# Kernel optimization log

Measured on AMD Instinct MI355X. Metric: run time of the kernel, lower is better.

The kernel has to match this reference:

```python
import jax, jax.numpy as jnp
import numpy as np

B, S, D, Q, N, H = 2, 2048, 4096, 32, 8, 128
ROPE_THETA = 10000.0


def apply_rope(x, positions, head_dim, theta):
    # x: [B, S, heads, H], positions: [B, S] int
    half = head_dim // 2
    inv_freq = 1.0 / (theta ** (jnp.arange(half, dtype=jnp.float32) * 2.0 / head_dim))
    angles = positions.astype(jnp.float32)[..., None] * inv_freq  # [B, S, half]
    cos = jnp.cos(angles)[:, :, None, :]  # [B, S, 1, half]
    sin = jnp.sin(angles)[:, :, None, :]
    x1, x2 = x[..., :half], x[..., half:]
    return jnp.concatenate([x1 * cos - x2 * sin, x2 * cos + x1 * sin], axis=-1).astype(x.dtype)


def setup_inputs() -> dict:
    key = jax.random.key(0)
    ks = jax.random.split(key, 5)
    x = jax.random.normal(ks[0], (B, S, D), dtype=jnp.float32)
    positions = jnp.broadcast_to(jnp.arange(S, dtype=jnp.int32)[None, :], (B, S))
    scale = 0.02
    Wq = jax.random.normal(ks[1], (Q, D, H), dtype=jnp.float32) * scale
    Wk = jax.random.normal(ks[2], (N, D, H), dtype=jnp.float32) * scale
    Wv = jax.random.normal(ks[3], (N, D, H), dtype=jnp.float32) * scale
    Wo = jax.random.normal(ks[4], (Q, H, D), dtype=jnp.float32) * scale
    return {"x": x, "positions": positions, "Wq": Wq, "Wk": Wk, "Wv": Wv, "Wo": Wo}


def reference(x, positions, Wq, Wk, Wv, Wo):
    # Prefill path: QKV proj + RoPE + GQA causal attention + O proj.
    head_repeats = Q // N
    q_BSQH = jnp.einsum('BSD,QDH->BSQH', x, Wq)
    q_BSQH = apply_rope(q_BSQH, positions, H, ROPE_THETA)
    k_BSNH = jnp.einsum('BSD,NDH->BSNH', x, Wk)
    k_BSNH = apply_rope(k_BSNH, positions, H, ROPE_THETA)
    v_BSNH = jnp.einsum('BSD,NDH->BSNH', x, Wv)
    # GQA head repeat
    k_BTQH = jnp.repeat(k_BSNH, head_repeats, axis=2) if head_repeats > 1 else k_BSNH
    v_BTQH = jnp.repeat(v_BSNH, head_repeats, axis=2) if head_repeats > 1 else v_BSNH
    scores_BQST = jnp.einsum('BSQH,BTQH->BQST', q_BSQH, k_BTQH) / jnp.sqrt(jnp.float32(H))
    causal = jnp.tril(jnp.ones((1, 1, S, S), dtype=jnp.bool_))
    scores_BQST = jnp.where(causal, scores_BQST, -jnp.inf)
    weights_BQST = jax.nn.softmax(scores_BQST, axis=-1)
    out_BSQH = jnp.einsum('BQST,BTQH->BSQH', weights_BQST, v_BTQH)
    o_BSD = jnp.einsum('BSQH,QHD->BSD', out_BSQH, Wo)
    return o_BSD
```

## Files before the change

### kernel.cpp

```cpp
#include <hip/hip_runtime.h>
#include <cstdint>
#include <cstddef>

#define B_  2
#define S_  2048
#define D_  4096
#define QH_ 32
#define NH_ 8
#define HD_ 128
#define MROWS (B_ * S_)
#define NQKV  (QH_ * HD_ + 2 * NH_ * HD_)
#define KOFF  (QH_ * HD_)
#define VOFF  (QH_ * HD_ + NH_ * HD_)

typedef __attribute__((ext_vector_type(8))) short bf16x8;
typedef __attribute__((ext_vector_type(4))) float f32x4;

__device__ __forceinline__ unsigned short f2bf(float f) {
    unsigned int u = __float_as_uint(f);
    return (unsigned short)((u + 0x7FFFu + ((u >> 16) & 1u)) >> 16);
}
__device__ __forceinline__ float bf2f(unsigned short h) { return __uint_as_float(((unsigned int)h) << 16); }

__device__ __forceinline__ void gl2lds16(const void* g, void* l) {
    __builtin_amdgcn_global_load_lds(
        (const __attribute__((address_space(1))) void*)g,
        (__attribute__((address_space(3))) void*)l, 16, 0, 0);
}

__global__ __launch_bounds__(256)
void convert_bf16_kernel(const float* __restrict__ in, unsigned short* __restrict__ out)
{
    const size_t i = ((size_t)blockIdx.x * 256 + threadIdx.x) * 8;
    float4 a = *(const float4*)(in + i);
    float4 b = *(const float4*)(in + i + 4);
    uint4 o;
    o.x = (unsigned int)f2bf(a.x) | ((unsigned int)f2bf(a.y) << 16);
    o.y = (unsigned int)f2bf(a.z) | ((unsigned int)f2bf(a.w) << 16);
    o.z = (unsigned int)f2bf(b.x) | ((unsigned int)f2bf(b.y) << 16);
    o.w = (unsigned int)f2bf(b.z) | ((unsigned int)f2bf(b.w) << 16);
    *(uint4*)(out + i) = o;
}

__global__ __launch_bounds__(256)
void transpose_conv_kernel(const float* __restrict__ in, unsigned short* __restrict__ out,
                           int R, int C)
{
    __shared__ unsigned short tile[64][72];
    const int t  = threadIdx.x;
    const int c0 = blockIdx.x * 64;
    const int r0 = blockIdx.y * 64;
    in  += (size_t)blockIdx.z * R * C;
    out += (size_t)blockIdx.z * R * C;
    {
        const int rr = t >> 4;
        const int cc = (t & 15) * 4;
        #pragma unroll
        for (int p = 0; p < 4; ++p) {
            float4 v = *(const float4*)(in + (size_t)(r0 + p * 16 + rr) * C + c0 + cc);
            unsigned int lo = (unsigned int)f2bf(v.x) | ((unsigned int)f2bf(v.y) << 16);
            unsigned int hi = (unsigned int)f2bf(v.z) | ((unsigned int)f2bf(v.w) << 16);
            *(uint2*)&tile[p * 16 + rr][cc] = make_uint2(lo, hi);
        }
    }
    __syncthreads();
    {
        const int j  = t >> 3;
        const int i8 = (t & 7) * 8;
        #pragma unroll
        for (int p = 0; p < 2; ++p) {
            unsigned short tmp[8];
            #pragma unroll
            for (int e = 0; e < 8; ++e) tmp[e] = tile[i8 + e][p * 32 + j];
            *(uint4*)(out + (size_t)(c0 + p * 32 + j) * R + r0 + i8) = *(uint4*)tmp;
        }
    }
}

__global__ __launch_bounds__(256)
void transpose_v_kernel(const unsigned short* __restrict__ qkv, unsigned short* __restrict__ vt)
{
    __shared__ unsigned short tile[64][76];
    const int t  = threadIdx.x;
    const int z  = blockIdx.z;
    const int b  = z >> 3, kh = z & 7;
    const int h0 = blockIdx.x * 64;
    const int s0 = blockIdx.y * 64;
    const unsigned short* in = qkv + (size_t)(b * S_) * NQKV + VOFF + kh * HD_;
    unsigned short* outb = vt + (size_t)z * HD_ * S_;
    {
        const int rr = t >> 4;
        const int cc = (t & 15) * 4;
        #pragma unroll
        for (int p = 0; p < 4; ++p) {
            uint2 v = *(const uint2*)(in + (size_t)(s0 + p * 16 + rr) * NQKV + h0 + cc);
            *(uint2*)&tile[p * 16 + rr][cc] = v;
        }
    }
    __syncthreads();
    {
        const int j  = t >> 3;
        const int i8 = (t & 7) * 8;
        #pragma unroll
        for (int p = 0; p < 2; ++p) {
            unsigned short tmp[8];
            #pragma unroll
            for (int e = 0; e < 8; ++e) tmp[e] = tile[i8 + e][p * 32 + j];
            *(uint4*)(outb + (size_t)(h0 + p * 32 + j) * S_ + s0 + i8) = *(uint4*)tmp;
        }
    }
}

template<int CF32>
__global__ __launch_bounds__(512, 2)
void gemm256_kernel(const unsigned short* __restrict__ A,
                    const unsigned short* __restrict__ Bt,
                    void* __restrict__ Cp, int Nst, int K)
{
    __shared__ alignas(16) unsigned short lds[3][2][256][32];

    const int t = threadIdx.x, l = t & 63, w = t >> 6;
    const int gx  = gridDim.x;
    const int nwg = gx * gridDim.y;
    int lin = blockIdx.y * gx + blockIdx.x;
    lin = (lin & 7) * (nwg >> 3) + (lin >> 3);
    const int bn = (lin % gx) * 256, bm = (lin / gx) * 256;
    const int wr = w >> 2, wc = w & 3;
    const int lm = l & 15, lg = l >> 4;

    f32x4 acc[8][4];
    #pragma unroll
    for (int i = 0; i < 8; ++i)
        #pragma unroll
        for (int j = 0; j < 4; ++j) acc[i][j] = (f32x4){0.f, 0.f, 0.f, 0.f};

    const int srow = w * 16 + (l >> 2);
    const int scol = (l & 3) * 8;
    const unsigned short* Asrc = A  + (size_t)(bm + srow) * K + scol;
    const unsigned short* Bsrc = Bt + (size_t)(bn + srow) * K + scol;

    #define STAGE_A(tt, bb) do {                                                  \
        gl2lds16(Asrc + (size_t)(tt) * 32,                  &lds[bb][0][w*16][0]); \
        gl2lds16(Asrc + (size_t)128*K + (size_t)(tt) * 32,  &lds[bb][0][128 + w*16][0]); } while (0)
    #define STAGE_B(tt, bb) do {                                                  \
        gl2lds16(Bsrc + (size_t)(tt) * 32,                  &lds[bb][1][w*16][0]); \
        gl2lds16(Bsrc + (size_t)128*K + (size_t)(tt) * 32,  &lds[bb][1][128 + w*16][0]); } while (0)

    const int nkt = K >> 5;
    STAGE_A(0, 0); STAGE_B(0, 0);
    STAGE_A(1, 1); STAGE_B(1, 1);

    for (int kt = 0; kt < nkt; ++kt) {
        if (kt + 1 < nkt) asm volatile("s_waitcnt vmcnt(4)" ::: "memory");
        else              asm volatile("s_waitcnt vmcnt(0)" ::: "memory");
        asm volatile("s_barrier" ::: "memory");

        const unsigned short (*bufA)[32] = lds[kt % 3][0];
        const unsigned short (*bufB)[32] = lds[kt % 3][1];
        const int nb = (kt + 2) % 3;

        bf16x8 bfr[4], afr[4];
        #pragma unroll
        for (int j = 0; j < 4; ++j) bfr[j] = *(const bf16x8*)&bufB[wc * 64 + j * 16 + lm][lg * 8];
        #pragma unroll
        for (int i = 0; i < 4; ++i) afr[i] = *(const bf16x8*)&bufA[wr * 128 + i * 16 + lm][lg * 8];
        if (kt + 2 < nkt) STAGE_A(kt + 2, nb);
        __builtin_amdgcn_s_setprio(1);
        #pragma unroll
        for (int i = 0; i < 4; ++i)
            #pragma unroll
            for (int j = 0; j < 4; ++j)
                acc[i][j] = __builtin_amdgcn_mfma_f32_16x16x32_bf16(afr[i], bfr[j], acc[i][j], 0, 0, 0);
        __builtin_amdgcn_s_setprio(0);
        asm volatile("s_barrier" ::: "memory");

        #pragma unroll
        for (int i = 0; i < 4; ++i) afr[i] = *(const bf16x8*)&bufA[wr * 128 + (i + 4) * 16 + lm][lg * 8];
        if (kt + 2 < nkt) STAGE_B(kt + 2, nb);
        __builtin_amdgcn_s_setprio(1);
        #pragma unroll
        for (int i = 0; i < 4; ++i)
            #pragma unroll
            for (int j = 0; j < 4; ++j)
                acc[i + 4][j] = __builtin_amdgcn_mfma_f32_16x16x32_bf16(afr[i], bfr[j], acc[i + 4][j], 0, 0, 0);
        __builtin_amdgcn_s_setprio(0);
    }
    #undef STAGE_A
    #undef STAGE_B

    const int lr4 = lg * 4;
    #pragma unroll
    for (int i = 0; i < 8; ++i) {
        #pragma unroll
        for (int j = 0; j < 4; ++j) {
            int row = bm + wr * 128 + i * 16 + lr4;
            int col = bn + wc * 64 + j * 16 + lm;
            #pragma unroll
            for (int jj = 0; jj < 4; ++jj) {
                if constexpr (CF32)
                    ((float*)Cp)[(size_t)(row + jj) * Nst + col] = acc[i][j][jj];
                else
                    ((unsigned short*)Cp)[(size_t)(row + jj) * Nst + col] = f2bf(acc[i][j][jj]);
            }
        }
    }
}

template<int LOG2H>
__global__ __launch_bounds__(256)
void rope_kernel(unsigned short* __restrict__ data, const int* __restrict__ positions)
{
    const int gid  = blockIdx.x * 256 + threadIdx.x;
    const int j    = gid & 63;
    const int hr   = gid >> 6;
    const int head = hr & ((1 << LOG2H) - 1);
    const int bs   = hr >> LOG2H;
    const float pos = (float)positions[bs];
    const float inv = expf(-0.14391156831f * (float)j);
    float s, c;
    sincosf(pos * inv, &s, &c);
    const size_t base = (size_t)bs * NQKV + head * HD_;
    const float x1 = bf2f(data[base + j]);
    const float x2 = bf2f(data[base + 64 + j]);
    data[base + j]      = f2bf(x1 * c - x2 * s);
    data[base + 64 + j] = f2bf(x2 * c + x1 * s);
}

__global__ __launch_bounds__(256)
void attn_kernel(const unsigned short* __restrict__ qkv,
                 const unsigned short* __restrict__ vt,
                 unsigned short* __restrict__ ao)
{
    constexpr int LDK = 136;
    constexpr int LDV = 72;
    __shared__ alignas(16) unsigned short k_s[64][LDK];
    __shared__ alignas(16) unsigned short v_t[128][LDV];
    __shared__ alignas(16) unsigned short p_s[4][16][LDV];

    const int t   = threadIdx.x;
    const int blk = blockIdx.x;
    const int sb  = 31 - (blk >> 6);
    const int pr  = blk & 63;
    const int qh  = pr >> 1;
    const int b   = pr & 1;
    const int kh  = qh >> 2;
    const int l   = t & 63, w = t >> 6;
    const int lm  = l & 15;
    const int lg  = l >> 4;
    const int lg4 = lg * 4;
    const int lko = lg * 8;
    const int wrow = w * 16 + lm;

    const unsigned short* vtb = vt + (size_t)(b * NH_ + kh) * HD_ * S_;

    bf16x8 qf[4];
    {
        const size_t qrow = (size_t)(b * S_ + sb * 64 + wrow) * NQKV + qh * HD_;
        #pragma unroll
        for (int kk = 0; kk < 4; ++kk)
            qf[kk] = *(const bf16x8*)(qkv + qrow + kk * 32 + lko);
    }

    f32x4 acc_o[8];
    #pragma unroll
    for (int i = 0; i < 8; ++i) acc_o[i] = (f32x4){0.f, 0.f, 0.f, 0.f};
    float mreg = -1e30f, lreg = 0.f;

    const float sm_scale = 0.08838834764831845f;

    for (int c = 0; c <= sb; ++c) {
        __syncthreads();
        {
            const int key = t >> 2, seg = t & 3;
            const size_t g = (size_t)(b * S_ + c * 64 + key) * NQKV + KOFF + kh * HD_ + seg * 32;
            const uint4* ksrc = (const uint4*)(qkv + g);
            #pragma unroll
            for (int i = 0; i < 4; ++i)
                *(uint4*)&k_s[key][seg * 32 + i * 8] = ksrc[i];
        }
        {
            const int h  = t >> 1;
            const int ko = (t & 1) * 32;
            const unsigned short* src = vtb + (size_t)h * S_ + c * 64 + ko;
            #pragma unroll
            for (int i = 0; i < 4; ++i)
                *(uint4*)&v_t[h][ko + i * 8] = *(const uint4*)(src + i * 8);
        }
        __syncthreads();

        f32x4 acc_s[4];
        #pragma unroll
        for (int t4 = 0; t4 < 4; ++t4) acc_s[t4] = (f32x4){0.f, 0.f, 0.f, 0.f};
        #pragma unroll
        for (int kk = 0; kk < 4; ++kk) {
            const bf16x8 qv = qf[kk];
            bf16x8 kf0 = *(const bf16x8*)&k_s[0 * 16 + lm][kk * 32 + lko];
            bf16x8 kf1 = *(const bf16x8*)&k_s[1 * 16 + lm][kk * 32 + lko];
            bf16x8 kf2 = *(const bf16x8*)&k_s[2 * 16 + lm][kk * 32 + lko];
            bf16x8 kf3 = *(const bf16x8*)&k_s[3 * 16 + lm][kk * 32 + lko];
            __builtin_amdgcn_s_setprio(1);
            acc_s[0] = __builtin_amdgcn_mfma_f32_16x16x32_bf16(kf0, qv, acc_s[0], 0, 0, 0);
            acc_s[1] = __builtin_amdgcn_mfma_f32_16x16x32_bf16(kf1, qv, acc_s[1], 0, 0, 0);
            acc_s[2] = __builtin_amdgcn_mfma_f32_16x16x32_bf16(kf2, qv, acc_s[2], 0, 0, 0);
            acc_s[3] = __builtin_amdgcn_mfma_f32_16x16x32_bf16(kf3, qv, acc_s[3], 0, 0, 0);
            __builtin_amdgcn_s_setprio(0);
        }

        const bool diag = (c == sb);
        float p[4][4];
        #pragma unroll
        for (int t4 = 0; t4 < 4; ++t4)
            #pragma unroll
            for (int r = 0; r < 4; ++r) {
                float s = acc_s[t4][r] * sm_scale;
                if (diag && (t4 * 16 + lg4 + r > wrow)) s = -1e30f;
                p[t4][r] = s;
            }
        float mc = p[0][0];
        #pragma unroll
        for (int t4 = 0; t4 < 4; ++t4)
            #pragma unroll
            for (int r = 0; r < 4; ++r) mc = fmaxf(mc, p[t4][r]);
        mc = fmaxf(mc, __shfl_xor(mc, 16, 64));
        mc = fmaxf(mc, __shfl_xor(mc, 32, 64));
        float sf = 1.0f;
        if (mc > mreg + 8.0f) {
            sf = __expf(mreg - mc);
            mreg = mc;
            lreg *= sf;
        }
        if (__any(sf != 1.0f)) {
            #pragma unroll
            for (int r = 0; r < 4; ++r) {
                const float s_r = __shfl(sf, (l & 48) | (lg4 + r), 64);
                #pragma unroll
                for (int ht = 0; ht < 8; ++ht) acc_o[ht][r] *= s_r;
            }
        }
        float ps = 0.f;
        #pragma unroll
        for (int t4 = 0; t4 < 4; ++t4)
            #pragma unroll
            for (int r = 0; r < 4; ++r) {
                p[t4][r] = __expf(p[t4][r] - mreg);
                ps += p[t4][r];
            }
        ps += __shfl_xor(ps, 16, 64);
        ps += __shfl_xor(ps, 32, 64);
        lreg += ps;
        #pragma unroll
        for (int t4 = 0; t4 < 4; ++t4) {
            unsigned int d0 = (unsigned int)f2bf(p[t4][0]) | ((unsigned int)f2bf(p[t4][1]) << 16);
            unsigned int d1 = (unsigned int)f2bf(p[t4][2]) | ((unsigned int)f2bf(p[t4][3]) << 16);
            *(unsigned int*)&p_s[w][lm][t4 * 16 + lg4]     = d0;
            *(unsigned int*)&p_s[w][lm][t4 * 16 + lg4 + 2] = d1;
        }

        #pragma unroll
        for (int kk = 0; kk < 2; ++kk) {
            const bf16x8 pa = *(const bf16x8*)&p_s[w][lm][kk * 32 + lko];
            #pragma unroll
            for (int ht = 0; ht < 8; ht += 4) {
                bf16x8 bv0 = *(const bf16x8*)&v_t[(ht + 0) * 16 + lm][kk * 32 + lko];
                bf16x8 bv1 = *(const bf16x8*)&v_t[(ht + 1) * 16 + lm][kk * 32 + lko];
                bf16x8 bv2 = *(const bf16x8*)&v_t[(ht + 2) * 16 + lm][kk * 32 + lko];
                bf16x8 bv3 = *(const bf16x8*)&v_t[(ht + 3) * 16 + lm][kk * 32 + lko];
                __builtin_amdgcn_s_setprio(1);
                acc_o[ht + 0] = __builtin_amdgcn_mfma_f32_16x16x32_bf16(pa, bv0, acc_o[ht + 0], 0, 0, 0);
                acc_o[ht + 1] = __builtin_amdgcn_mfma_f32_16x16x32_bf16(pa, bv1, acc_o[ht + 1], 0, 0, 0);
                acc_o[ht + 2] = __builtin_amdgcn_mfma_f32_16x16x32_bf16(pa, bv2, acc_o[ht + 2], 0, 0, 0);
                acc_o[ht + 3] = __builtin_amdgcn_mfma_f32_16x16x32_bf16(pa, bv3, acc_o[ht + 3], 0, 0, 0);
                __builtin_amdgcn_s_setprio(0);
            }
        }
    }

    #pragma unroll
    for (int r = 0; r < 4; ++r) {
        const float lr = __shfl(lreg, (l & 48) | (lg4 + r), 64);
        const float invl = 1.f / lr;
        const size_t row = (size_t)(b * S_ + sb * 64 + w * 16 + lg4 + r);
        #pragma unroll
        for (int ht = 0; ht < 8; ++ht)
            ao[(row * QH_ + qh) * HD_ + ht * 16 + lm] = f2bf(acc_o[ht][r] * invl);
    }
}

extern "C" void kernel_launch(void* const* d_in, const int* in_sizes, int n_in,
                              void* d_out, int out_size, void* d_ws, size_t ws_size,
                              hipStream_t stream)
{
    const float* x  = (const float*)d_in[0];
    const int*  pos = (const int*)d_in[1];
    const float* Wq = (const float*)d_in[2];
    const float* Wk = (const float*)d_in[3];
    const float* Wv = (const float*)d_in[4];
    const float* Wo = (const float*)d_in[5];
    float* out = (float*)d_out;

    char* wsb = (char*)d_ws;
    unsigned short* qkv = (unsigned short*)(wsb);
    unsigned short* wt  = (unsigned short*)(wsb + 50331648);
    unsigned short* vt  = (unsigned short*)(wsb + 83886080);
    unsigned short* r0  = (unsigned short*)(wsb + 100663296);

    const dim3 blk(256);
    const dim3 blk512(512);
    convert_bf16_kernel<<<8192, blk, 0, stream>>>(x, r0);
    transpose_conv_kernel<<<dim3(2, 64, 32), blk, 0, stream>>>(Wq, wt, D_, HD_);
    transpose_conv_kernel<<<dim3(2, 64, 8),  blk, 0, stream>>>(Wk, wt + (size_t)KOFF * D_, D_, HD_);
    transpose_conv_kernel<<<dim3(2, 64, 8),  blk, 0, stream>>>(Wv, wt + (size_t)VOFF * D_, D_, HD_);
    gemm256_kernel<0><<<dim3(NQKV / 256, MROWS / 256), blk512, 0, stream>>>(r0, wt, qkv, NQKV, D_);
    transpose_conv_kernel<<<dim3(64, 64, 1), blk, 0, stream>>>(Wo, wt, D_, D_);
    transpose_v_kernel<<<dim3(2, 32, 16), blk, 0, stream>>>(qkv, vt);
    rope_kernel<5><<<(MROWS * QH_ * 64) / 256, blk, 0, stream>>>(qkv, pos);
    rope_kernel<3><<<(MROWS * NH_ * 64) / 256, blk, 0, stream>>>(qkv + KOFF, pos);
    attn_kernel<<<B_ * QH_ * (S_ / 64), blk, 0, stream>>>(qkv, vt, r0);
    gemm256_kernel<1><<<dim3(D_ / 256, MROWS / 256), blk512, 0, stream>>>(r0, wt, out, D_, QH_ * HD_);
}
```

Before: 607.2 us.

## Rewrite GEMM as 8-phase ping-pong pipeline with 64-wide K tiles and swizzled LDS

```diff
diff --git a/kernel.cpp b/kernel.cpp
--- a/kernel.cpp
+++ b/kernel.cpp
@@ -113,11 +113,12 @@
 
 template<int CF32>
 __global__ __launch_bounds__(512, 2)
-void gemm256_kernel(const unsigned short* __restrict__ A,
-                    const unsigned short* __restrict__ Bt,
-                    void* __restrict__ Cp, int Nst, int K)
-{
-    __shared__ alignas(16) unsigned short lds[3][2][256][32];
+void gemm8p_kernel(const unsigned short* __restrict__ A,
+                   const unsigned short* __restrict__ Bt,
+                   void* __restrict__ Cp, int Nst, int K)
+{
+    __shared__ alignas(16) unsigned short Al[2][2][128][64];
+    __shared__ alignas(16) unsigned short Bl[2][2][128][64];
 
     const int t = threadIdx.x, l = t & 63, w = t >> 6;
     const int gx  = gridDim.x;
@@ -128,73 +129,134 @@
     const int wr = w >> 2, wc = w & 3;
     const int lm = l & 15, lg = l >> 4;
 
+    const int sk  = ((lm >> 2) & 1) << 5;
+    const int kc0 = sk + lg * 8;
+    const int kc1 = (sk ^ 32) + lg * 8;
+
     f32x4 acc[8][4];
     #pragma unroll
     for (int i = 0; i < 8; ++i)
         #pragma unroll
         for (int j = 0; j < 4; ++j) acc[i][j] = (f32x4){0.f, 0.f, 0.f, 0.f};
 
-    const int srow = w * 16 + (l >> 2);
-    const int scol = (l & 3) * 8;
-    const unsigned short* Asrc = A  + (size_t)(bm + srow) * K + scol;
-    const unsigned short* Bsrc = Bt + (size_t)(bn + srow) * K + scol;
-
-    #define STAGE_A(tt, bb) do {                                                  \
-        gl2lds16(Asrc + (size_t)(tt) * 32,                  &lds[bb][0][w*16][0]); \
-        gl2lds16(Asrc + (size_t)128*K + (size_t)(tt) * 32,  &lds[bb][0][128 + w*16][0]); } while (0)
-    #define STAGE_B(tt, bb) do {                                                  \
-        gl2lds16(Bsrc + (size_t)(tt) * 32,                  &lds[bb][1][w*16][0]); \
-        gl2lds16(Bsrc + (size_t)128*K + (size_t)(tt) * 32,  &lds[bb][1][128 + w*16][0]); } while (0)
-
-    const int nkt = K >> 5;
-    STAGE_A(0, 0); STAGE_B(0, 0);
-    STAGE_A(1, 1); STAGE_B(1, 1);
+    const int srow = w * 8 + (l >> 3);
+    const int scol = (((l & 7) ^ (((l >> 5) & 1) << 2))) * 8;
+    const unsigned short* Ag = A  + (size_t)(bm + srow) * K + scol;
+    const unsigned short* Bg = Bt + (size_t)(bn + srow) * K + scol;
+
+    #define STG_A(bb, hh, ko) do { \
+        gl2lds16(Ag + (size_t)((hh) * 128) * K + (ko),      &Al[bb][hh][w * 8][0]);      \
+        gl2lds16(Ag + (size_t)((hh) * 128 + 64) * K + (ko), &Al[bb][hh][64 + w * 8][0]); } while (0)
+    #define STG_B(bb, hh, ko) do { \
+        gl2lds16(Bg + (size_t)((hh) * 128) * K + (ko),      &Bl[bb][hh][w * 8][0]);      \
+        gl2lds16(Bg + (size_t)((hh) * 128 + 64) * K + (ko), &Bl[bb][hh][64 + w * 8][0]); } while (0)
+
+    const int nkt = K >> 6;
+    STG_A(0, 0, 0); STG_B(0, 0, 0); STG_B(0, 1, 0); STG_A(0, 1, 0);
+    asm volatile("s_waitcnt vmcnt(4)" ::: "memory");
+    asm volatile("s_barrier" ::: "memory");
+
+    bf16x8 af[4][2], bfp[2][2];
 
     for (int kt = 0; kt < nkt; ++kt) {
-        if (kt + 1 < nkt) asm volatile("s_waitcnt vmcnt(4)" ::: "memory");
-        else              asm volatile("s_waitcnt vmcnt(0)" ::: "memory");
-        asm volatile("s_barrier" ::: "memory");
-
-        const unsigned short (*bufA)[32] = lds[kt % 3][0];
-        const unsigned short (*bufB)[32] = lds[kt % 3][1];
-        const int nb = (kt + 2) % 3;
-
-        bf16x8 bfr[4], afr[4];
-        #pragma unroll
-        for (int j = 0; j < 4; ++j) bfr[j] = *(const bf16x8*)&bufB[wc * 64 + j * 16 + lm][lg * 8];
-        #pragma unroll
-        for (int i = 0; i < 4; ++i) afr[i] = *(const bf16x8*)&bufA[wr * 128 + i * 16 + lm][lg * 8];
-        if (kt + 2 < nkt) STAGE_A(kt + 2, nb);
+        const int cur = kt & 1, nxt = cur ^ 1;
+        const bool pf = (kt + 1 < nkt);
+        const size_t ko = (size_t)(kt + 1) * 64;
+        const unsigned short (*Ac0)[64] = Al[cur][0];
+        const unsigned short (*Ac1)[64] = Al[cur][1];
+        const unsigned short (*Bc0)[64] = Bl[cur][0];
+        const unsigned short (*Bc1)[64] = Bl[cur][1];
+
+        #pragma unroll
+        for (int i = 0; i < 4; ++i) {
+            af[i][0] = *(const bf16x8*)&Ac0[wr * 16 + i * 32 + lm][kc0];
+            af[i][1] = *(const bf16x8*)&Ac0[wr * 16 + i * 32 + lm][kc1];
+        }
+        #pragma unroll
+        for (int j = 0; j < 2; ++j) {
+            bfp[j][0] = *(const bf16x8*)&Bc0[j * 64 + wc * 16 + lm][kc0];
+            bfp[j][1] = *(const bf16x8*)&Bc0[j * 64 + wc * 16 + lm][kc1];
+        }
+        if (pf) STG_A(nxt, 0, ko);
+        asm volatile("s_barrier" ::: "memory");
         __builtin_amdgcn_s_setprio(1);
         #pragma unroll
         for (int i = 0; i < 4; ++i)
             #pragma unroll
-            for (int j = 0; j < 4; ++j)
-                acc[i][j] = __builtin_amdgcn_mfma_f32_16x16x32_bf16(afr[i], bfr[j], acc[i][j], 0, 0, 0);
+            for (int j = 0; j < 2; ++j) {
+                acc[i][j] = __builtin_amdgcn_mfma_f32_16x16x32_bf16(af[i][0], bfp[j][0], acc[i][j], 0, 0, 0);
+                acc[i][j] = __builtin_amdgcn_mfma_f32_16x16x32_bf16(af[i][1], bfp[j][1], acc[i][j], 0, 0, 0);
+            }
         __builtin_amdgcn_s_setprio(0);
-        asm volatile("s_barrier" ::: "memory");
-
-        #pragma unroll
-        for (int i = 0; i < 4; ++i) afr[i] = *(const bf16x8*)&bufA[wr * 128 + (i + 4) * 16 + lm][lg * 8];
-        if (kt + 2 < nkt) STAGE_B(kt + 2, nb);
+        asm volatile("s_waitcnt vmcnt(4)" ::: "memory");
+        asm volatile("s_barrier" ::: "memory");
+
+        #pragma unroll
+        for (int j = 0; j < 2; ++j) {
+            bfp[j][0] = *(const bf16x8*)&Bc1[j * 64 + wc * 16 + lm][kc0];
+            bfp[j][1] = *(const bf16x8*)&Bc1[j * 64 + wc * 16 + lm][kc1];
+        }
+        if (pf) STG_B(nxt, 0, ko);
+        asm volatile("s_barrier" ::: "memory");
         __builtin_amdgcn_s_setprio(1);
         #pragma unroll
         for (int i = 0; i < 4; ++i)
             #pragma unroll
-            for (int j = 0; j < 4; ++j)
-                acc[i + 4][j] = __builtin_amdgcn_mfma_f32_16x16x32_bf16(afr[i], bfr[j], acc[i + 4][j], 0, 0, 0);
+            for (int j = 0; j < 2; ++j) {
+                acc[i][j + 2] = __builtin_amdgcn_mfma_f32_16x16x32_bf16(af[i][0], bfp[j][0], acc[i][j + 2], 0, 0, 0);
+                acc[i][j + 2] = __builtin_amdgcn_mfma_f32_16x16x32_bf16(af[i][1], bfp[j][1], acc[i][j + 2], 0, 0, 0);
+            }
         __builtin_amdgcn_s_setprio(0);
-    }
-    #undef STAGE_A
-    #undef STAGE_B
+        asm volatile("s_waitcnt vmcnt(4)" ::: "memory");
+        asm volatile("s_barrier" ::: "memory");
+
+        #pragma unroll
+        for (int i = 0; i < 4; ++i) {
+            af[i][0] = *(const bf16x8*)&Ac1[wr * 16 + i * 32 + lm][kc0];
+            af[i][1] = *(const bf16x8*)&Ac1[wr * 16 + i * 32 + lm][kc1];
+        }
+        if (pf) STG_B(nxt, 1, ko);
+        asm volatile("s_barrier" ::: "memory");
+        __builtin_amdgcn_s_setprio(1);
+        #pragma unroll
+        for (int i = 0; i < 4; ++i)
+            #pragma unroll
+            for (int j = 0; j < 2; ++j) {
+                acc[i + 4][j + 2] = __builtin_amdgcn_mfma_f32_16x16x32_bf16(af[i][0], bfp[j][0], acc[i + 4][j + 2], 0, 0, 0);
+                acc[i + 4][j + 2] = __builtin_amdgcn_mfma_f32_16x16x32_bf16(af[i][1], bfp[j][1], acc[i + 4][j + 2], 0, 0, 0);
+            }
+        __builtin_amdgcn_s_setprio(0);
+        asm volatile("s_barrier" ::: "memory");
+
+        #pragma unroll
+        for (int j = 0; j < 2; ++j) {
+            bfp[j][0] = *(const bf16x8*)&Bc0[j * 64 + wc * 16 + lm][kc0];
+            bfp[j][1] = *(const bf16x8*)&Bc0[j * 64 + wc * 16 + lm][kc1];
+        }
+        if (pf) STG_A(nxt, 1, ko);
+        asm volatile("s_barrier" ::: "memory");
+        __builtin_amdgcn_s_setprio(1);
+        #pragma unroll
+        for (int i = 0; i < 4; ++i)
+            #pragma unroll
+            for (int j = 0; j < 2; ++j) {
+                acc[i + 4][j] = __builtin_amdgcn_mfma_f32_16x16x32_bf16(af[i][0], bfp[j][0], acc[i + 4][j], 0, 0, 0);
+                acc[i + 4][j] = __builtin_amdgcn_mfma_f32_16x16x32_bf16(af[i][1], bfp[j][1], acc[i + 4][j], 0, 0, 0);
+            }
+        __builtin_amdgcn_s_setprio(0);
+        asm volatile("s_waitcnt vmcnt(4)" ::: "memory");
+        asm volatile("s_barrier" ::: "memory");
+    }
+    #undef STG_A
+    #undef STG_B
 
     const int lr4 = lg * 4;
     #pragma unroll
     for (int i = 0; i < 8; ++i) {
         #pragma unroll
         for (int j = 0; j < 4; ++j) {
-            int row = bm + wr * 128 + i * 16 + lr4;
-            int col = bn + wc * 64 + j * 16 + lm;
+            int row = bm + wr * 16 + i * 32 + lr4;
+            int col = bn + wc * 16 + j * 64 + lm;
             #pragma unroll
             for (int jj = 0; jj < 4; ++jj) {
                 if constexpr (CF32)
@@ -410,11 +472,11 @@
     transpose_conv_kernel<<<dim3(2, 64, 32), blk, 0, stream>>>(Wq, wt, D_, HD_);
     transpose_conv_kernel<<<dim3(2, 64, 8),  blk, 0, stream>>>(Wk, wt + (size_t)KOFF * D_, D_, HD_);
     transpose_conv_kernel<<<dim3(2, 64, 8),  blk, 0, stream>>>(Wv, wt + (size_t)VOFF * D_, D_, HD_);
-    gemm256_kernel<0><<<dim3(NQKV / 256, MROWS / 256), blk512, 0, stream>>>(r0, wt, qkv, NQKV, D_);
+    gemm8p_kernel<0><<<dim3(NQKV / 256, MROWS / 256), blk512, 0, stream>>>(r0, wt, qkv, NQKV, D_);
     transpose_conv_kernel<<<dim3(64, 64, 1), blk, 0, stream>>>(Wo, wt, D_, D_);
     transpose_v_kernel<<<dim3(2, 32, 16), blk, 0, stream>>>(qkv, vt);
     rope_kernel<5><<<(MROWS * QH_ * 64) / 256, blk, 0, stream>>>(qkv, pos);
     rope_kernel<3><<<(MROWS * NH_ * 64) / 256, blk, 0, stream>>>(qkv + KOFF, pos);
     attn_kernel<<<B_ * QH_ * (S_ / 64), blk, 0, stream>>>(qkv, vt, r0);
-    gemm256_kernel<1><<<dim3(D_ / 256, MROWS / 256), blk512, 0, stream>>>(r0, wt, out, D_, QH_ * HD_);
-}
+    gemm8p_kernel<1><<<dim3(D_ / 256, MROWS / 256), blk512, 0, stream>>>(r0, wt, out, D_, QH_ * HD_);
+}
```

Result: slower. 626.0 us (+3.1%).
